# Kernel optimization log

Hardware: AMD Instinct MI355X
Metric: run time of the kernel (lower is better)

Reference implementation:

```python
import jax, jax.numpy as jnp
import numpy as np

B, S, T = 512, 1024, 48
START, STOP, PAD = 45, 46, 47
NEG = -10000.0


def setup_inputs() -> dict:
    key = jax.random.key(0)
    k1, k2, k3, k4 = jax.random.split(key, 4)
    feats = jax.random.normal(k1, (B, S, T), dtype=jnp.float32)
    # contiguous-prefix masks (lengths in [1, S]) as the torch code assumes
    lengths = jax.random.randint(k2, (B,), 1, S + 1)
    masks = (jnp.arange(S)[None, :] < lengths[:, None]).astype(jnp.float32)
    tags = jax.random.randint(k3, (B, S), 0, T - 3)  # real tags only
    # transitions[i, j] = score of transitioning from tag j to tag i
    trans = jax.random.normal(k4, (T, T), dtype=jnp.float32)
    trans = trans.at[START, :].set(NEG)
    trans = trans.at[:, STOP].set(NEG)
    trans = trans.at[:, PAD].set(NEG)
    trans = trans.at[PAD, :].set(NEG)
    trans = trans.at[PAD, STOP].set(0.0)
    trans = trans.at[PAD, PAD].set(0.0)
    return {"feats": feats, "masks": masks, "tags": tags, "transitions": trans}


def _forward_algo(feats, masks, transitions):
    # feats [B,S,T], masks [B,S] -> partition log Z per sequence [B]
    score0 = jnp.full(feats.shape[::2], NEG, dtype=feats.dtype).at[:, START].set(0.0)

    def step(score, xs):
        emit, m = xs  # emit [B,T], m [B,1]
        # new[b,i] = LSE_j(score[b,j] + trans[i,j]) + emit[b,i]
        new = jax.nn.logsumexp(score[:, None, :] + transitions[None, :, :], axis=2) + emit
        return new * m + score * (1.0 - m), None

    xs = (jnp.swapaxes(feats, 0, 1), masks.T[:, :, None])
    score, _ = jax.lax.scan(step, score0, xs)
    return jax.nn.logsumexp(score + transitions[STOP][None, :], axis=1)


def _score_sentence(feats, masks, tags, transitions):
    # gold path score, vectorized over batch and time
    Bb = masks.shape[0]
    tags_ext = jnp.concatenate(
        [jnp.full((Bb, 1), START, dtype=tags.dtype), tags], axis=1)  # [B,S+1]
    emission = jnp.take_along_axis(feats, tags[:, :, None], axis=2)[:, :, 0]  # [B,S]
    trans_sc = transitions[tags_ext[:, 1:], tags_ext[:, :-1]]  # [B,S]
    score = jnp.sum((emission + trans_sc) * masks, axis=1)
    last_idx = masks.sum(1).astype(jnp.int32)  # length -> index into tags_ext
    last_tags = jnp.take_along_axis(tags_ext, last_idx[:, None], axis=1)[:, 0]
    return score + transitions[STOP, last_tags]


def reference(feats, masks, tags, transitions):
    # standard CRF negative log-likelihood per sequence: logZ - gold score
    return _forward_algo(feats, masks, transitions) - _score_sentence(
        feats, masks, tags, transitions)
```

## Files before the change

kernel.cpp:

```cpp
#include <hip/hip_runtime.h>
#include <cstdint>

constexpr int Sd = 1024;
constexpr int Td = 48;
constexpr int NTAG = 45;
constexpr int START_ = 45;
constexpr int STOP_ = 46;

__device__ __forceinline__ int rfl_i(int x) { return __builtin_amdgcn_readfirstlane(x); }

#define FMD(acc, s, ee, N) \
    asm("v_fmac_f32 %0, %1, %2 row_ror:" #N " row_mask:0xf bank_mask:0xf" \
        : "+v"(acc) : "v"(s), "v"(ee))
#define MULD(acc, s, ee, N) \
    asm("v_mul_f32 %0, %1, %2 row_ror:" #N " row_mask:0xf bank_mask:0xf" \
        : "=v"(acc) : "v"(s), "v"(ee))

#define SLOT16(s, E, aA, aB) do {                                              \
    aA = (s) * E[0];                                                           \
    FMD(aA, s, E[1], 1);  FMD(aA, s, E[2], 2);  FMD(aA, s, E[3], 3);           \
    FMD(aA, s, E[4], 4);  FMD(aA, s, E[5], 5);  FMD(aA, s, E[6], 6);           \
    FMD(aA, s, E[7], 7);                                                       \
    MULD(aB, s, E[8], 8);                                                      \
    FMD(aB, s, E[9], 9);  FMD(aB, s, E[10], 10); FMD(aB, s, E[11], 11);        \
    FMD(aB, s, E[12], 12); FMD(aB, s, E[13], 13); FMD(aB, s, E[14], 14);       \
    FMD(aB, s, E[15], 15);                                                     \
} while (0)

#define STEP1(PF) do {                                                         \
    int _vi = __float_as_int(v);                                               \
    int _b1 = __builtin_amdgcn_ds_bpermute(a16, _vi);                          \
    int _b2 = __builtin_amdgcn_ds_bpermute(a32, _vi);                          \
    float _s1 = __int_as_float(_b1), _s2 = __int_as_float(_b2);                \
    float a0A, a0B, a1A, a1B, a2A, a2B;                                        \
    SLOT16(v,   eA0, a0A, a0B);                                                \
    SLOT16(_s1, eA1, a1A, a1B);                                                \
    SLOT16(_s2, eA2, a2A, a2B);                                                \
    float tot_ = ((a0A + a0B) + (a1A + a1B)) + (a2A + a2B);                    \
    L += kx;                                                                   \
    uf = tot_ * sc;                                                            \
    v  = tot_ * ((PF) * sc);                                                   \
    { int _kb = rfl_i(__float_as_int(v));                                      \
      kx = ((_kb >> 23) & 0xFF) - 127;                                         \
      sc = __int_as_float((127 - kx) << 23); }                                 \
} while (0)

#define ADVP() do {                                                            \
    bool ok_ = isb ? (tn > 0) : (tn < tmax);                                   \
    pcur += ok_ ? sAdv : 0;                                                    \
    tn   += ok_ ? sInc : 0;                                                    \
} while (0)

__launch_bounds__(64, 1)
__global__ void crf_chains(const float* __restrict__ feats,
                           const float* __restrict__ masks,
                           const int* __restrict__ tags,
                           const float* __restrict__ trans,
                           float* __restrict__ wsv,
                           float* __restrict__ wsu,
                           int* __restrict__ wsLF, int* __restrict__ wsLB,
                           float* __restrict__ wsg,
                           int Bn)
{
    __shared__ float tl[Td * Td];
    const int lane = threadIdx.x;
    const bool isb = ((int)blockIdx.x >= Bn);
    const int b = isb ? ((int)blockIdx.x - Bn) : (int)blockIdx.x;

    for (int i = lane; i < Td * Td; i += 64) tl[i] = trans[i];
    __syncthreads();

    const size_t bS = (size_t)b * Sd;

    float c = 0.f;
    for (int t = lane; t < Sd; t += 64) c += masks[bS + t];
#pragma unroll
    for (int off = 32; off; off >>= 1) c += __shfl_xor(c, off);
    int len = (int)(c + 0.5f);
    if (len < 1) len = 1;
    len = rfl_i(len);

    if (!isb) {
        float g = 0.f;
        for (int t = lane; t < len; t += 64) {
            const int tag  = tags[bS + t];
            const int prev = (t == 0) ? START_ : tags[bS + t - 1];
            g += feats[(bS + t) * Td + tag] + tl[tag * Td + prev];
        }
#pragma unroll
        for (int off = 32; off; off >>= 1) g += __shfl_xor(g, off);
        g += tl[STOP_ * Td + tags[bS + len - 1]];
        if (lane == 0) wsg[b] = g;
    }

    const int p = lane & 15;
    const int qd = __builtin_amdgcn_mov_dpp(p, 0x121, 0xF, 0xF, false);
    const int d = (qd == ((p + 1) & 15)) ? 1 : -1;
    const int r0 = (lane >> 4) & 3;

    const int a16 = (((lane + 16) % Td) << 2);
    const int a32 = (((lane + 32) % Td) << 2);

    float eA0[16], eA1[16], eA2[16];
#pragma unroll
    for (int h = 0; h < 3; ++h) {
        float* dst = (h == 0) ? eA0 : (h == 1) ? eA1 : eA2;
        const int blk = 16 * ((r0 + h) % 3);
#pragma unroll
        for (int i = 0; i < 16; ++i) {
            const int cc = blk + ((p + d * i) & 15);
            float e0 = 0.f;
            if (!isb) {
                if (lane < NTAG) e0 = __expf(tl[lane * Td + cc]);
            } else {
                if (lane < Td)   e0 = __expf(tl[cc * Td + lane]);
            }
            dst[i] = e0;
        }
    }

    const int lidx = (lane < Td) ? lane : 0;
    const float* frow = feats + bS * Td;
    const int Fh = (len + 1) >> 1;
    const int act = rfl_i(isb ? (len - Fh) : (Fh - 1));
    const int it0 = isb ? (len - 1) : 0;

    float einit;
    if (!isb) einit = (lane < NTAG) ? __expf(tl[lane * Td + START_]) : 0.f;
    else      einit = (lane < Td)   ? __expf(tl[STOP_ * Td + lane])  : 0.f;

    float v  = __expf(frow[(size_t)it0 * Td + lidx]) * einit;
    float uf = einit;
    int L = 0, kx; float sc;
    { int kb = rfl_i(__float_as_int(v)); kx = ((kb >> 23) & 0xFF) - 127;
      sc = __int_as_float((127 - kx) << 23); }

    auto eidx0 = [&](int s) -> int {
        if (!isb) { int t = 1 + s; return t < Sd ? t : (Sd - 1); }
        int t = len - 2 - s; return t > 0 ? t : 0;
    };
    float pf0 = __expf(frow[(size_t)eidx0(0) * Td + lidx]);
    float pf1 = __expf(frow[(size_t)eidx0(1) * Td + lidx]);
    float pf2 = __expf(frow[(size_t)eidx0(2) * Td + lidx]);
    float pf3 = __expf(frow[(size_t)eidx0(3) * Td + lidx]);
    float pf4 = __expf(frow[(size_t)eidx0(4) * Td + lidx]);
    float pf5 = __expf(frow[(size_t)eidx0(5) * Td + lidx]);
    float pf6 = __expf(frow[(size_t)eidx0(6) * Td + lidx]);
    float pf7 = __expf(frow[(size_t)eidx0(7) * Td + lidx]);
    int tn = eidx0(8);
    const float* pcur = frow + (size_t)tn * Td;
    const int sAdv = isb ? -Td : Td;
    const int sInc = isb ? -1 : 1;
    const int tmax = Sd - 1;

    int s = 0;
    while (s + 8 <= act) {
        STEP1(pf0); pf0 = __expf(pcur[lidx]); ADVP();
        STEP1(pf1); pf1 = __expf(pcur[lidx]); ADVP();
        STEP1(pf2); pf2 = __expf(pcur[lidx]); ADVP();
        STEP1(pf3); pf3 = __expf(pcur[lidx]); ADVP();
        STEP1(pf4); pf4 = __expf(pcur[lidx]); ADVP();
        STEP1(pf5); pf5 = __expf(pcur[lidx]); ADVP();
        STEP1(pf6); pf6 = __expf(pcur[lidx]); ADVP();
        STEP1(pf7); pf7 = __expf(pcur[lidx]); ADVP();
        s += 8;
    }
    if (s < act) { STEP1(pf0); ++s; }
    if (s < act) { STEP1(pf1); ++s; }
    if (s < act) { STEP1(pf2); ++s; }
    if (s < act) { STEP1(pf3); ++s; }
    if (s < act) { STEP1(pf4); ++s; }
    if (s < act) { STEP1(pf5); ++s; }
    if (s < act) { STEP1(pf6); ++s; }

    if (!isb) {
        if (lane < Td) wsv[lane * Bn + b] = v;
        if (lane == 0) wsLF[b] = L;
    } else {
        if (lane < Td) wsu[lane * Bn + b] = uf;
        if (lane == 0) wsLB[b] = L;
    }
}

__launch_bounds__(64)
__global__ void crf_combine(const float* __restrict__ wsv,
                            const float* __restrict__ wsu,
                            const int* __restrict__ wsLF,
                            const int* __restrict__ wsLB,
                            const float* __restrict__ wsg,
                            float* __restrict__ out, int Bn)
{
    const int b = blockIdx.x * 64 + threadIdx.x;
    if (b >= Bn) return;
    float dot = 0.f;
#pragma unroll
    for (int j = 0; j < Td; ++j)
        dot += wsv[j * Bn + b] * wsu[j * Bn + b];
    const float ln2 = 0.6931471805599453f;
    out[b] = (float)(wsLF[b] + wsLB[b]) * ln2 + __logf(dot) - wsg[b];
}

extern "C" void kernel_launch(void* const* d_in, const int* in_sizes, int n_in,
                              void* d_out, int out_size, void* d_ws, size_t ws_size,
                              hipStream_t stream) {
    const float* feats = (const float*)d_in[0];
    const float* masks = (const float*)d_in[1];
    const int*   tags  = (const int*)d_in[2];
    const float* trans = (const float*)d_in[3];
    float* outp = (float*)d_out;

    const int Bn = in_sizes[1] / Sd;

    float* wsv  = (float*)d_ws;
    float* wsu  = wsv + (size_t)Td * Bn;
    int*   wsLF = (int*)(wsu + (size_t)Td * Bn);
    int*   wsLB = wsLF + Bn;
    float* wsg  = (float*)(wsLB + Bn);

    crf_chains<<<dim3(2 * Bn), dim3(64), 0, stream>>>(feats, masks, tags, trans,
                                                      wsv, wsu, wsLF, wsLB, wsg, Bn);
    crf_combine<<<dim3((Bn + 63) / 64), dim3(64), 0, stream>>>(wsv, wsu, wsLF, wsLB, wsg, outp, Bn);
}
```

Measured before the change: 119.1 us.

## Interleave two independent CRF chains per wavefront to hide latency

Each wavefront now runs the forward (or backward) recurrence for two batch elements at once, interleaving their steps so that the serial dependency chain of one (bpermute, DPP FMAs, readfirstlane) overlaps with the other. The grid is halved, the prefetch depth per chain drops from 8 to 4, and a tail loop finishes whichever chain is longer. The kernel keeps one shared transition-weight register set, but register pressure rises, the launch-bounds occupancy hint changes, and time spent on the longer chain's tail runs without a partner to overlap with.

```diff
diff --git a/kernel.cpp b/kernel.cpp
--- a/kernel.cpp
+++ b/kernel.cpp
@@ -27,31 +27,32 @@
     FMD(aB, s, E[15], 15);                                                     \
 } while (0)
 
-#define STEP1(PF) do {                                                         \
-    int _vi = __float_as_int(v);                                               \
+#define STEPC(vv, uff, kxx, scc, LL, PF) do {                                  \
+    int _vi = __float_as_int(vv);                                              \
     int _b1 = __builtin_amdgcn_ds_bpermute(a16, _vi);                          \
     int _b2 = __builtin_amdgcn_ds_bpermute(a32, _vi);                          \
     float _s1 = __int_as_float(_b1), _s2 = __int_as_float(_b2);                \
     float a0A, a0B, a1A, a1B, a2A, a2B;                                        \
-    SLOT16(v,   eA0, a0A, a0B);                                                \
-    SLOT16(_s1, eA1, a1A, a1B);                                                \
-    SLOT16(_s2, eA2, a2A, a2B);                                                \
+    SLOT16(vv,  eE0, a0A, a0B);                                                \
+    SLOT16(_s1, eE1, a1A, a1B);                                                \
+    SLOT16(_s2, eE2, a2A, a2B);                                                \
     float tot_ = ((a0A + a0B) + (a1A + a1B)) + (a2A + a2B);                    \
-    L += kx;                                                                   \
-    uf = tot_ * sc;                                                            \
-    v  = tot_ * ((PF) * sc);                                                   \
-    { int _kb = rfl_i(__float_as_int(v));                                      \
-      kx = ((_kb >> 23) & 0xFF) - 127;                                         \
-      sc = __int_as_float((127 - kx) << 23); }                                 \
+    LL += kxx;                                                                 \
+    uff = tot_ * scc;                                                          \
+    vv = tot_ * ((PF) * scc);                                                  \
+    { int _kb = rfl_i(__float_as_int(vv));                                     \
+      kxx = ((_kb >> 23) & 0xFF) - 127;                                        \
+      scc = __int_as_float((127 - kxx) << 23); }                               \
 } while (0)
 
-#define ADVP() do {                                                            \
-    bool ok_ = isb ? (tn > 0) : (tn < tmax);                                   \
-    pcur += ok_ ? sAdv : 0;                                                    \
-    tn   += ok_ ? sInc : 0;                                                    \
-} while (0)
-
-__launch_bounds__(64, 1)
+#define ADVA() do { bool ok_ = isb ? (tnA > 0) : (tnA < Sd - 1);               \
+    pcA += ok_ ? sAdv : 0; tnA += ok_ ? sInc : 0; } while (0)
+#define ADVB() do { bool ok_ = isb ? (tnB > 0) : (tnB < Sd - 1);               \
+    pcB += ok_ ? sAdv : 0; tnB += ok_ ? sInc : 0; } while (0)
+#define ADVT() do { bool ok_ = isb ? (tnT > 0) : (tnT < Sd - 1);               \
+    pcT += ok_ ? sAdv : 0; tnT += ok_ ? sInc : 0; } while (0)
+
+__launch_bounds__(64)
 __global__ void crf_chains(const float* __restrict__ feats,
                            const float* __restrict__ masks,
                            const int* __restrict__ tags,
@@ -64,33 +65,43 @@
 {
     __shared__ float tl[Td * Td];
     const int lane = threadIdx.x;
-    const bool isb = ((int)blockIdx.x >= Bn);
-    const int b = isb ? ((int)blockIdx.x - Bn) : (int)blockIdx.x;
+    const int nPair = Bn >> 1;
+    const bool isb = ((int)blockIdx.x >= nPair);
+    const int pair = isb ? ((int)blockIdx.x - nPair) : (int)blockIdx.x;
+    const int bA = pair * 2, bB = bA + 1;
 
     for (int i = lane; i < Td * Td; i += 64) tl[i] = trans[i];
     __syncthreads();
 
-    const size_t bS = (size_t)b * Sd;
-
-    float c = 0.f;
-    for (int t = lane; t < Sd; t += 64) c += masks[bS + t];
-#pragma unroll
-    for (int off = 32; off; off >>= 1) c += __shfl_xor(c, off);
-    int len = (int)(c + 0.5f);
-    if (len < 1) len = 1;
-    len = rfl_i(len);
+    const size_t bSA = (size_t)bA * Sd;
+    const size_t bSB = (size_t)bB * Sd;
+
+    auto get_len = [&](size_t bS) {
+        float c = 0.f;
+        for (int t = lane; t < Sd; t += 64) c += masks[bS + t];
+#pragma unroll
+        for (int off = 32; off; off >>= 1) c += __shfl_xor(c, off);
+        int l = (int)(c + 0.5f);
+        return rfl_i(l < 1 ? 1 : l);
+    };
+    const int lenA = get_len(bSA);
+    const int lenB = get_len(bSB);
 
     if (!isb) {
-        float g = 0.f;
-        for (int t = lane; t < len; t += 64) {
-            const int tag  = tags[bS + t];
-            const int prev = (t == 0) ? START_ : tags[bS + t - 1];
-            g += feats[(bS + t) * Td + tag] + tl[tag * Td + prev];
-        }
-#pragma unroll
-        for (int off = 32; off; off >>= 1) g += __shfl_xor(g, off);
-        g += tl[STOP_ * Td + tags[bS + len - 1]];
-        if (lane == 0) wsg[b] = g;
+        auto get_gold = [&](size_t bS, int len) {
+            float g = 0.f;
+            for (int t = lane; t < len; t += 64) {
+                const int tag  = tags[bS + t];
+                const int prev = (t == 0) ? START_ : tags[bS + t - 1];
+                g += feats[(bS + t) * Td + tag] + tl[tag * Td + prev];
+            }
+#pragma unroll
+            for (int off = 32; off; off >>= 1) g += __shfl_xor(g, off);
+            return g + tl[STOP_ * Td + tags[bS + len - 1]];
+        };
+        const float gA = get_gold(bSA, lenA);
+        const float gB = get_gold(bSB, lenB);
+        if (lane == 0) { wsg[bA] = gA; wsg[bB] = gB; }
     }
 
     const int p = lane & 15;
@@ -101,84 +112,122 @@
     const int a16 = (((lane + 16) % Td) << 2);
     const int a32 = (((lane + 32) % Td) << 2);
 
-    float eA0[16], eA1[16], eA2[16];
+    float eE0[16], eE1[16], eE2[16];
 #pragma unroll
     for (int h = 0; h < 3; ++h) {
-        float* dst = (h == 0) ? eA0 : (h == 1) ? eA1 : eA2;
+        float* dst = (h == 0) ? eE0 : (h == 1) ? eE1 : eE2;
         const int blk = 16 * ((r0 + h) % 3);
 #pragma unroll
         for (int i = 0; i < 16; ++i) {
             const int cc = blk + ((p + d * i) & 15);
             float e0 = 0.f;
-            if (!isb) {
-                if (lane < NTAG) e0 = __expf(tl[lane * Td + cc]);
-            } else {
-                if (lane < Td)   e0 = __expf(tl[cc * Td + lane]);
-            }
+            if (!isb) { if (lane < NTAG) e0 = __expf(tl[lane * Td + cc]); }
+            else      { if (lane < Td)   e0 = __expf(tl[cc * Td + lane]); }
             dst[i] = e0;
         }
     }
 
     const int lidx = (lane < Td) ? lane : 0;
-    const float* frow = feats + bS * Td;
-    const int Fh = (len + 1) >> 1;
-    const int act = rfl_i(isb ? (len - Fh) : (Fh - 1));
-    const int it0 = isb ? (len - 1) : 0;
+    const float* frowA = feats + bSA * Td;
+    const float* frowB = feats + bSB * Td;
+    const int FhA = (lenA + 1) >> 1, FhB = (lenB + 1) >> 1;
+    const int actA = rfl_i(isb ? (lenA - FhA) : (FhA - 1));
+    const int actB = rfl_i(isb ? (lenB - FhB) : (FhB - 1));
 
     float einit;
     if (!isb) einit = (lane < NTAG) ? __expf(tl[lane * Td + START_]) : 0.f;
     else      einit = (lane < Td)   ? __expf(tl[STOP_ * Td + lane])  : 0.f;
 
-    float v  = __expf(frow[(size_t)it0 * Td + lidx]) * einit;
-    float uf = einit;
-    int L = 0, kx; float sc;
-    { int kb = rfl_i(__float_as_int(v)); kx = ((kb >> 23) & 0xFF) - 127;
-      sc = __int_as_float((127 - kx) << 23); }
-
-    auto eidx0 = [&](int s) -> int {
-        if (!isb) { int t = 1 + s; return t < Sd ? t : (Sd - 1); }
-        int t = len - 2 - s; return t > 0 ? t : 0;
+    const int itA = isb ? (lenA - 1) : 0;
+    const int itB = isb ? (lenB - 1) : 0;
+    float vA = __expf(frowA[(size_t)itA * Td + lidx]) * einit;
+    float vB = __expf(frowB[(size_t)itB * Td + lidx]) * einit;
+    float ufA = einit, ufB = einit;
+    int LA = 0, LB = 0, kxA, kxB; float scA, scB;
+    { int kb = rfl_i(__float_as_int(vA)); kxA = ((kb >> 23) & 0xFF) - 127;
+      scA = __int_as_float((127 - kxA) << 23); }
+    { int kb = rfl_i(__float_as_int(vB)); kxB = ((kb >> 23) & 0xFF) - 127;
+      scB = __int_as_float((127 - kxB) << 23); }
+
+    auto eiA = [&](int s) -> int {
+        if (isb) { int t = lenA - 2 - s; return t > 0 ? t : 0; }
+        int t = 1 + s; return t < Sd ? t : (Sd - 1);
     };
-    float pf0 = __expf(frow[(size_t)eidx0(0) * Td + lidx]);
-    float pf1 = __expf(frow[(size_t)eidx0(1) * Td + lidx]);
-    float pf2 = __expf(frow[(size_t)eidx0(2) * Td + lidx]);
-    float pf3 = __expf(frow[(size_t)eidx0(3) * Td + lidx]);
-    float pf4 = __expf(frow[(size_t)eidx0(4) * Td + lidx]);
-    float pf5 = __expf(frow[(size_t)eidx0(5) * Td + lidx]);
-    float pf6 = __expf(frow[(size_t)eidx0(6) * Td + lidx]);
-    float pf7 = __expf(frow[(size_t)eidx0(7) * Td + lidx]);
-    int tn = eidx0(8);
-    const float* pcur = frow + (size_t)tn * Td;
+    auto eiB = [&](int s) -> int {
+        if (isb) { int t = lenB - 2 - s; return t > 0 ? t : 0; }
+        int t = 1 + s; return t < Sd ? t : (Sd - 1);
+    };
+    float pfA0 = __expf(frowA[(size_t)eiA(0) * Td + lidx]);
+    float pfA1 = __expf(frowA[(size_t)eiA(1) * Td + lidx]);
+    float pfA2 = __expf(frowA[(size_t)eiA(2) * Td + lidx]);
+    float pfA3 = __expf(frowA[(size_t)eiA(3) * Td + lidx]);
+    float pfB0 = __expf(frowB[(size_t)eiB(0) * Td + lidx]);
+    float pfB1 = __expf(frowB[(size_t)eiB(1) * Td + lidx]);
+    float pfB2 = __expf(frowB[(size_t)eiB(2) * Td + lidx]);
+    float pfB3 = __expf(frowB[(size_t)eiB(3) * Td + lidx]);
+    int tnA = eiA(4), tnB = eiB(4);
+    const float* pcA = frowA + (size_t)tnA * Td;
+    const float* pcB = frowB + (size_t)tnB * Td;
     const int sAdv = isb ? -Td : Td;
     const int sInc = isb ? -1 : 1;
-    const int tmax = Sd - 1;
-
-    int s = 0;
-    while (s + 8 <= act) {
-        STEP1(pf0); pf0 = __expf(pcur[lidx]); ADVP();
-        STEP1(pf1); pf1 = __expf(pcur[lidx]); ADVP();
-        STEP1(pf2); pf2 = __expf(pcur[lidx]); ADVP();
-        STEP1(pf3); pf3 = __expf(pcur[lidx]); ADVP();
-        STEP1(pf4); pf4 = __expf(pcur[lidx]); ADVP();
-        STEP1(pf5); pf5 = __expf(pcur[lidx]); ADVP();
-        STEP1(pf6); pf6 = __expf(pcur[lidx]); ADVP();
-        STEP1(pf7); pf7 = __expf(pcur[lidx]); ADVP();
-        s += 8;
-    }
-    if (s < act) { STEP1(pf0); ++s; }
-    if (s < act) { STEP1(pf1); ++s; }
-    if (s < act) { STEP1(pf2); ++s; }
-    if (s < act) { STEP1(pf3); ++s; }
-    if (s < act) { STEP1(pf4); ++s; }
-    if (s < act) { STEP1(pf5); ++s; }
-    if (s < act) { STEP1(pf6); ++s; }
+
+    const int common = actA < actB ? actA : actB;
+    int k = 0;
+    while (k + 4 <= common) {
+        STEPC(vA, ufA, kxA, scA, LA, pfA0); STEPC(vB, ufB, kxB, scB, LB, pfB0);
+        pfA0 = __expf(pcA[lidx]); ADVA();   pfB0 = __expf(pcB[lidx]); ADVB();
+        STEPC(vA, ufA, kxA, scA, LA, pfA1); STEPC(vB, ufB, kxB, scB, LB, pfB1);
+        pfA1 = __expf(pcA[lidx]); ADVA();   pfB1 = __expf(pcB[lidx]); ADVB();
+        STEPC(vA, ufA, kxA, scA, LA, pfA2); STEPC(vB, ufB, kxB, scB, LB, pfB2);
+        pfA2 = __expf(pcA[lidx]); ADVA();   pfB2 = __expf(pcB[lidx]); ADVB();
+        STEPC(vA, ufA, kxA, scA, LA, pfA3); STEPC(vB, ufB, kxB, scB, LB, pfB3);
+        pfA3 = __expf(pcA[lidx]); ADVA();   pfB3 = __expf(pcB[lidx]); ADVB();
+        k += 4;
+    }
+    if (k < common) { STEPC(vA, ufA, kxA, scA, LA, pfA0); STEPC(vB, ufB, kxB, scB, LB, pfB0); ++k; }
+    if (k < common) { STEPC(vA, ufA, kxA, scA, LA, pfA1); STEPC(vB, ufB, kxB, scB, LB, pfB1); ++k; }
+    if (k < common) { STEPC(vA, ufA, kxA, scA, LA, pfA2); STEPC(vB, ufB, kxB, scB, LB, pfB2); ++k; }
+
+    const bool longA = actA > actB;
+    const int actT = longA ? actA : actB;
+    if (common < actT) {
+        const float* frowT = longA ? frowA : frowB;
+        const int lenT = longA ? lenA : lenB;
+        float vT = longA ? vA : vB;
+        float ufT = longA ? ufA : ufB;
+        int kxT = longA ? kxA : kxB; float scT = longA ? scA : scB;
+        int LT = longA ? LA : LB;
+        auto eiT = [&](int s) -> int {
+            if (isb) { int t = lenT - 2 - s; return t > 0 ? t : 0; }
+            int t = 1 + s; return t < Sd ? t : (Sd - 1);
+        };
+        float pfT0 = __expf(frowT[(size_t)eiT(common + 0) * Td + lidx]);
+        float pfT1 = __expf(frowT[(size_t)eiT(common + 1) * Td + lidx]);
+        float pfT2 = __expf(frowT[(size_t)eiT(common + 2) * Td + lidx]);
+        float pfT3 = __expf(frowT[(size_t)eiT(common + 3) * Td + lidx]);
+        int tnT = eiT(common + 4);
+        const float* pcT = frowT + (size_t)tnT * Td;
+        int kT = common;
+        while (kT + 4 <= actT) {
+            STEPC(vT, ufT, kxT, scT, LT, pfT0); pfT0 = __expf(pcT[lidx]); ADVT();
+            STEPC(vT, ufT, kxT, scT, LT, pfT1); pfT1 = __expf(pcT[lidx]); ADVT();
+            STEPC(vT, ufT, kxT, scT, LT, pfT2); pfT2 = __expf(pcT[lidx]); ADVT();
+            STEPC(vT, ufT, kxT, scT, LT, pfT3); pfT3 = __expf(pcT[lidx]); ADVT();
+            kT += 4;
+        }
+        if (kT < actT) { STEPC(vT, ufT, kxT, scT, LT, pfT0); ++kT; }
+        if (kT < actT) { STEPC(vT, ufT, kxT, scT, LT, pfT1); ++kT; }
+        if (kT < actT) { STEPC(vT, ufT, kxT, scT, LT, pfT2); ++kT; }
+        if (longA) { vA = vT; ufA = ufT; LA = LT; }
+        else       { vB = vT; ufB = ufT; LB = LT; }
+    }
 
     if (!isb) {
-        if (lane < Td) wsv[lane * Bn + b] = v;
-        if (lane == 0) wsLF[b] = L;
+        if (lane < Td) { wsv[lane * Bn + bA] = vA; wsv[lane * Bn + bB] = vB; }
+        if (lane == 0) { wsLF[bA] = LA; wsLF[bB] = LB; }
     } else {
-        if (lane < Td) wsu[lane * Bn + b] = uf;
-        if (lane == 0) wsLB[b] = L;
+        if (lane < Td) { wsu[lane * Bn + bA] = ufA; wsu[lane * Bn + bB] = ufB; }
+        if (lane == 0) { wsLB[bA] = LA; wsLB[bB] = LB; }
     }
 }
 
@@ -217,7 +266,7 @@
     int*   wsLB = wsLF + Bn;
     float* wsg  = (float*)(wsLB + Bn);
 
-    crf_chains<<<dim3(2 * Bn), dim3(64), 0, stream>>>(feats, masks, tags, trans,
-                                                      wsv, wsu, wsLF, wsLB, wsg, Bn);
+    crf_chains<<<dim3(Bn), dim3(64), 0, stream>>>(feats, masks, tags, trans,
+                                                  wsv, wsu, wsLF, wsLB, wsg, Bn);
     crf_combine<<<dim3((Bn + 63) / 64), dim3(64), 0, stream>>>(wsv, wsu, wsLF, wsLB, wsg, outp, Bn);
 }
```

New measurement: 242.2 us. +103.4%, slower.
